# Performance work log

Measured on AMD Instinct MI355X. Metric: run time of the kernel, lower is better.

The kernel has to match this reference:

```python
import jax, jax.numpy as jnp
import numpy as np

NUM_HEADS = 8
WINDOW = (2, 8, 8)
NW = 64  # number of distinct window masks
TOPK = 2  # selected_n + 1


def _rel_position_index(ws):
    d, h, w = ws
    coords = np.stack(np.meshgrid(np.arange(d), np.arange(h), np.arange(w), indexing='ij'))  # (3,d,h,w)
    flat = coords.reshape(3, -1)  # (3,N)
    rel = flat[:, :, None] - flat[:, None, :]  # (3,N,N)
    rel = rel.transpose(1, 2, 0).astype(np.int64)
    rel[..., 0] += d - 1
    rel[..., 1] += h - 1
    rel[..., 2] += w - 1
    rel[..., 0] *= (2 * h - 1) * (2 * w - 1)
    rel[..., 1] *= 2 * w - 1
    return jnp.asarray(rel.sum(-1), dtype=jnp.int32)  # (N,N)


def setup_inputs() -> dict:
    key = jax.random.key(0)
    ks = jax.random.split(key, 7)
    B_, N, C = 1024, 128, 128
    x = jax.random.normal(ks[0], (B_, N, C), jnp.float32)
    mask = jax.random.normal(ks[1], (NW, N, N), jnp.float32)
    Wq = jax.random.normal(ks[2], (C, C), jnp.float32) * 0.02
    Wkv = jax.random.normal(ks[3], (C, 2 * C), jnp.float32) * 0.02
    Wproj = jax.random.normal(ks[4], (C, C), jnp.float32) * 0.02
    bproj = jnp.zeros((C,), jnp.float32)
    tbl_len = (2 * WINDOW[0] - 1) * (2 * WINDOW[1] - 1) * (2 * WINDOW[2] - 1)  # 675
    bias_table = jax.random.normal(ks[5], (tbl_len, NUM_HEADS), jnp.float32) * 0.02
    rel_index = _rel_position_index(WINDOW)
    return dict(x=x, mask=mask, Wq=Wq, Wkv=Wkv, Wproj=Wproj, bproj=bproj,
                bias_table=bias_table, rel_index=rel_index)


def reference(x, mask, Wq, Wkv, Wproj, bproj, bias_table, rel_index):
    B_, N, C = x.shape
    h = NUM_HEADS
    hd = C // h
    scale = hd ** -0.5
    # q/k/v projections (qkv_bias=False)
    q = (x @ Wq).reshape(B_, N, h, hd).transpose(0, 2, 1, 3)            # (B_,h,N,hd)
    kv = (x @ Wkv).reshape(B_, N, 2, h, hd).transpose(2, 0, 3, 1, 4)    # (2,B_,h,N,hd)
    k, v = kv[0], kv[1]
    attn = jnp.einsum('bhnd,bhmd->bhnm', q * scale, k)                  # (B_,h,N,N)
    # gathered relative-position bias
    bias = bias_table[rel_index.reshape(-1)].reshape(N, N, h).transpose(2, 0, 1)
    attn = attn + bias[None]
    nW = mask.shape[0]
    attn = attn.reshape(B_ // nW, nW, h, N, N) + mask[None, :, None]
    attn = jax.nn.softmax(attn.reshape(B_, h, N, N), axis=-1)
    # only_one branch: top-k gather + weighted sum over V
    sv, si = jax.lax.top_k(attn, TOPK)                                  # (B_,h,N,K)
    sel = jnp.take_along_axis(v, si.reshape(B_, h, N * TOPK)[..., None], axis=2)
    sel = sel.reshape(B_, h, N, TOPK, hd)
    out = (sel * sv[..., None]).sum(axis=3)                             # (B_,h,N,hd)
    xo = out.transpose(0, 2, 1, 3).reshape(B_, N, C)
    return xo @ Wproj + bproj
```

## Files before the change

### kernel.cpp

```cpp
#include <hip/hip_runtime.h>
#include <hip/hip_bf16.h>
#include <stdint.h>

typedef __attribute__((ext_vector_type(8))) short short8;
typedef __attribute__((ext_vector_type(4))) float floatx4;

#define B_TOT 1024
#define N_TOK 128
#define C_DIM 128
#define NHEAD 8
#define NW_MASK 64

#define BIAS_OFF 0
#define WALL_OFF 524288
#define WHEAD_BYTES 30464
#define WPT_OFF 768000
#define WS_BYTES 800768

#define QS_LDS 0
#define KS_LDS 14336
#define VS_LDS 28672
#define XO_LDS 37376
#define WB_LDS 47616
#define WPTB_LDS 109056
#define LDS_BYTES 125440

#define MFMA(a, b, c) __builtin_amdgcn_mfma_f32_16x16x32_bf16((a), (b), (c), 0, 0, 0)

__device__ __forceinline__ float bf2f(ushort u) {
  union { uint32_t u; float f; } v; v.u = ((uint32_t)u) << 16; return v.f;
}
__device__ __forceinline__ ushort f2bf(float f) {
  uint32_t u = __float_as_uint(f);
  return (ushort)((u + 0x7FFFu + ((u >> 16) & 1u)) >> 16);
}
__device__ __forceinline__ void split3(float f, ushort& h, ushort& m, ushort& l) {
  h = f2bf(f);  float r  = f - bf2f(h);
  m = f2bf(r);  float r2 = r - bf2f(m);
  l = f2bf(r2);
}
__device__ __forceinline__ void split3t(float f, ushort& h, ushort& m, ushort& l) {
  h = (ushort)(__float_as_uint(f) >> 16);
  float r  = f - bf2f(h);
  m = (ushort)(__float_as_uint(r) >> 16);
  float r2 = r - bf2f(m);
  l = f2bf(r2);
}

__device__ __forceinline__ void dma16(const void* g, void* l_) {
  __builtin_amdgcn_global_load_lds((const __attribute__((address_space(1))) void*)g,
                                   (__attribute__((address_space(3))) void*)l_,
                                   16, 0, 0);
}

__global__ __launch_bounds__(512)
void prep_kernel(const int* __restrict__ rel_index, const float* __restrict__ table,
                 const float* __restrict__ Wq, const float* __restrict__ Wkv,
                 const float* __restrict__ Wproj, char* __restrict__ ws) {
  float*  bias_g = (float*)(ws + BIAS_OFF);
  ushort* wpt_g  = (ushort*)(ws + WPT_OFF);

  int idx = blockIdx.x * 512 + threadIdx.x;
  if (idx < 131072) {
    int h = idx >> 14, mn = idx & 16383;
    bias_g[idx] = table[rel_index[mn] * NHEAD + h];
  } else if (idx < 131072 + 16384) {
    int t = idx - 131072;
    int h = t >> 11, r = t & 2047, oc = r >> 7, kk = r & 127;
    ushort a, bb, cc;
    split3(Wq[kk * C_DIM + h * 16 + oc] * 0.25f, a, bb, cc);
    ushort* wqp = (ushort*)(ws + WALL_OFF + h * WHEAD_BYTES);
    wqp[0 * 2176 + oc * 136 + kk] = a;
    wqp[1 * 2176 + oc * 136 + kk] = bb;
    wqp[2 * 2176 + oc * 136 + kk] = cc;
  } else if (idx < 131072 + 2 * 16384) {
    int t = idx - 131072 - 16384;
    int h = t >> 11, r = t & 2047, oc = r >> 7, kk = r & 127;
    ushort a, bb, cc;
    split3(Wkv[kk * (2 * C_DIM) + h * 16 + oc], a, bb, cc);
    ushort* wkp = (ushort*)(ws + WALL_OFF + h * WHEAD_BYTES) + 6528;
    wkp[0 * 2176 + oc * 136 + kk] = a;
    wkp[1 * 2176 + oc * 136 + kk] = bb;
    wkp[2 * 2176 + oc * 136 + kk] = cc;
  } else if (idx < 131072 + 3 * 16384) {
    int t = idx - 131072 - 2 * 16384;
    int h = t >> 11, r = t & 2047, oc = r >> 7, kk = r & 127;
    ushort* wvp = (ushort*)(ws + WALL_OFF + h * WHEAD_BYTES) + 13056;
    wvp[oc * 136 + kk] = f2bf(Wkv[kk * (2 * C_DIM) + C_DIM + h * 16 + oc]);
  } else if (idx < 131072 + 4 * 16384) {
    int t = idx - 131072 - 3 * 16384;
    int hp = t >> 12, r = t & 4095, n = r >> 5, kk = r & 31;
    wpt_g[t] = f2bf(Wproj[(hp * 32 + kk) * C_DIM + n]);
  }
}

__global__ __launch_bounds__(512, 2)
void wattn_kernel(const float* __restrict__ x, const float* __restrict__ mask,
                  const float* __restrict__ bproj, const char* __restrict__ ws,
                  float* __restrict__ out) {
  extern __shared__ char smem[];
  ushort* qs = (ushort*)(smem + QS_LDS);
  ushort* ks = (ushort*)(smem + KS_LDS);
  float*  vs = (float*)(smem + VS_LDS);
  ushort* xo = (ushort*)(smem + XO_LDS);

  const float* bias_g = (const float*)(ws + BIAS_OFF);

  const int tid  = threadIdx.x;
  const int w    = tid >> 6;
  const int l    = tid & 63;
  const int quad = l >> 4;
  const int c    = l & 15;
  const int b    = blockIdx.x;
  const int wi   = b & (NW_MASK - 1);

  {
    const char* src = ws + WALL_OFF;
    char* dst = smem + WB_LDS;
    #pragma unroll
    for (int t = 0; t < 4; ++t) {
      int ch = t * 8 + w;
      if (ch < 30) dma16(src + ch * 1024 + l * 16, dst + ch * 1024 + l * 16);
    }
    dma16(ws + WPT_OFF + w * 1024 + l * 16, smem + WPTB_LDS + w * 1024 + l * 16);
  }

  short8 A1[8], A3[8];
  {
    const float* xrow = x + ((size_t)b * N_TOK + 16 * w + c) * C_DIM;
    #pragma unroll
    for (int kt = 0; kt < 8; ++kt) {
      int colb = kt * 16 + (quad & 1) * 8;
      floatx4 xa  = *(const floatx4*)(xrow + colb);
      floatx4 xb2 = *(const floatx4*)(xrow + colb + 4);
      short8 hi8, mi8, lo8;
      #pragma unroll
      for (int jj = 0; jj < 8; ++jj) {
        float f = (jj < 4) ? xa[jj] : xb2[jj - 4];
        ushort hh, mm, ll; split3t(f, hh, mm, ll);
        hi8[jj] = (short)hh; mi8[jj] = (short)mm; lo8[jj] = (short)ll;
      }
      A1[kt] = (quad < 2) ? hi8 : mi8;
      A3[kt] = (quad < 2) ? hi8 : lo8;
    }
  }

  floatx4 oacc[8];
  #pragma unroll
  for (int j = 0; j < 8; ++j) oacc[j] = (floatx4){0.f, 0.f, 0.f, 0.f};

  asm volatile("s_waitcnt vmcnt(0)" ::: "memory");
  __syncthreads();

  for (int h = 0; h < NHEAD; ++h) {
    if (h < 7) {
      const char* src = ws + WALL_OFF + (h + 1) * WHEAD_BYTES;
      char* dst = smem + WB_LDS + ((h + 1) & 1) * 30720;
      #pragma unroll
      for (int t = 0; t < 4; ++t) {
        int ch = t * 8 + w;
        if (ch < 30) dma16(src + ch * 1024 + l * 16, dst + ch * 1024 + l * 16);
      }
      if (h & 1) {
        int np = (h + 1) >> 1;
        dma16(ws + WPT_OFF + np * 8192 + w * 1024 + l * 16,
              smem + WPTB_LDS + (np & 1) * 8192 + w * 1024 + l * 16);
      }
    }

    {
      floatx4 aq = (floatx4){0.f,0.f,0.f,0.f};
      floatx4 ak = (floatx4){0.f,0.f,0.f,0.f};
      floatx4 av = (floatx4){0.f,0.f,0.f,0.f};
      const ushort* wh  = (const ushort*)(smem + WB_LDS + (h & 1) * 30720);
      const ushort* wqp = wh + c * 136;
      const ushort* wkp = wh + 6528 + c * 136;
      const ushort* wvp = wh + 13056 + c * 136;
      const int q3off = (quad < 2) ? 2 * 2176 : 0;
      #pragma unroll
      for (int kt = 0; kt < 8; ++kt) {
        int colb = kt * 16 + (quad & 1) * 8;
        short8 bq1 = *(const short8*)(wqp + colb);
        short8 bq2 = *(const short8*)(wqp + 2176 + colb);
        short8 bq3 = *(const short8*)(wqp + q3off + colb);
        aq = MFMA(A1[kt], bq1, aq);  aq = MFMA(A1[kt], bq2, aq);  aq = MFMA(A3[kt], bq3, aq);
        short8 bk1 = *(const short8*)(wkp + colb);
        short8 bk2 = *(const short8*)(wkp + 2176 + colb);
        short8 bk3 = *(const short8*)(wkp + q3off + colb);
        ak = MFMA(A1[kt], bk1, ak);  ak = MFMA(A1[kt], bk2, ak);  ak = MFMA(A3[kt], bk3, ak);
        short8 bv1 = *(const short8*)(wvp + colb);
        av = MFMA(A1[kt], bv1, av);
      }
      #pragma unroll
      for (int i = 0; i < 4; ++i) {
        int tok = 16 * w + 4 * quad + i;
        ushort a, bb, cc;
        split3t(aq[i], a, bb, cc);
        qs[tok * 56 + c] = a; qs[tok * 56 + 16 + c] = bb; qs[tok * 56 + 32 + c] = cc;
        split3t(ak[i], a, bb, cc);
        ks[tok * 56 + c] = a; ks[tok * 56 + 16 + c] = bb; ks[tok * 56 + 32 + c] = cc;
        vs[tok * 17 + c] = av[i];
      }
    }
    __syncthreads();

    {
      const ushort* qrow = qs + (16 * w + c) * 56;
      short8 aq1 = *(const short8*)(qrow + quad * 8);
      short8 aq3 = *(const short8*)(qrow + ((quad < 2) ? quad * 8 : 16 + quad * 8));

      float m1[4], m2[4], psum[4];
      int   i1[4], i2[4];

      #pragma unroll
      for (int j = 0; j < 8; ++j) {
        floatx4 acc;
        #pragma unroll
        for (int i = 0; i < 4; ++i) {
          int m = 16 * w + 4 * quad + i;
          int n = 16 * j + c;
          acc[i] = bias_g[(h * N_TOK + m) * N_TOK + n] +
                   mask[(wi * N_TOK + m) * N_TOK + n];
        }
        const ushort* krow = ks + (16 * j + c) * 56;
        int bo1 = (quad & 1) * 8;
        short8 b1 = *(const short8*)(krow + bo1);
        short8 b2 = *(const short8*)(krow + 16 + bo1);
        short8 b3 = *(const short8*)(krow + ((quad < 2) ? 32 + quad * 8
                                                        : (quad - 2) * 8));
        acc = MFMA(aq1, b1, acc);
        acc = MFMA(aq1, b2, acc);
        acc = MFMA(aq3, b3, acc);

        if (j == 0) {
          #pragma unroll
          for (int i = 0; i < 4; ++i) {
            m1[i] = acc[i]; i1[i] = c;
            m2[i] = -__builtin_inff(); i2[i] = -1;
            psum[i] = 1.0f;
          }
        } else {
          #pragma unroll
          for (int i = 0; i < 4; ++i) {
            float v = acc[i]; int col = 16 * j + c;
            bool g1 = v > m1[i];
            float e = __expf(g1 ? (m1[i] - v) : (v - m1[i]));
            psum[i] = g1 ? (psum[i] * e + 1.0f) : (psum[i] + e);
            bool g2 = (!g1) && (v > m2[i]);
            m2[i] = g1 ? m1[i] : (g2 ? v : m2[i]);
            i2[i] = g1 ? i1[i] : (g2 ? col : i2[i]);
            m1[i] = g1 ? v : m1[i];
            i1[i] = g1 ? col : i1[i];
          }
        }
      }

      #pragma unroll
      for (int i = 0; i < 4; ++i) {
        float M1 = m1[i], M2 = m2[i], PS = psum[i];
        int I1 = i1[i], I2 = i2[i];
        #pragma unroll
        for (int d = 1; d < 16; d <<= 1) {
          float om1 = __shfl_xor(M1, d); int oi1 = __shfl_xor(I1, d);
          float om2 = __shfl_xor(M2, d); int oi2 = __shfl_xor(I2, d);
          float ops = __shfl_xor(PS, d);
          bool aw = (M1 > om1) || (M1 == om1 && I1 < oi1);
          float M  = aw ? M1 : om1;  int I  = aw ? I1 : oi1;
          float lv = aw ? om1 : M1;  int li = aw ? oi1 : I1;
          float sv = aw ? M2 : om2;  int si = aw ? I2 : oi2;
          bool sb = (sv > lv) || (sv == lv && si < li);
          float e = __expf(lv - M);
          PS = (aw ? PS : ops) + (aw ? ops : PS) * e;
          M1 = M; I1 = I;
          M2 = sb ? sv : lv; I2 = sb ? si : li;
        }
        float p1 = 1.0f / PS;
        float p2 = __expf(M2 - M1) * p1;
        int tok = 16 * w + 4 * quad + i;
        float o = p1 * vs[I1 * 17 + c] + p2 * vs[I2 * 17 + c];
        xo[tok * 40 + (h & 1) * 16 + c] = f2bf(o);
      }
    }

    if (h & 1) {
      const ushort* wptp = (const ushort*)(smem + WPTB_LDS + ((h >> 1) & 1) * 8192);
      short8 a = *(const short8*)(xo + (16 * w + c) * 40 + quad * 8);
      #pragma unroll
      for (int j = 0; j < 8; ++j) {
        short8 bf = *(const short8*)(wptp + (16 * j + c) * 32 + quad * 8);
        oacc[j] = MFMA(a, bf, oacc[j]);
      }
    }
    __syncthreads();
  }

  #pragma unroll
  for (int j = 0; j < 8; ++j) {
    float bp = bproj[16 * j + c];
    #pragma unroll
    for (int i = 0; i < 4; ++i) {
      int row = 16 * w + 4 * quad + i;
      out[((size_t)b * N_TOK + row) * C_DIM + 16 * j + c] = oacc[j][i] + bp;
    }
  }
}

extern "C" void kernel_launch(void* const* d_in, const int* in_sizes, int n_in,
                              void* d_out, int out_size, void* d_ws, size_t ws_size,
                              hipStream_t stream) {
  const float* x     = (const float*)d_in[0];
  const float* mask  = (const float*)d_in[1];
  const float* Wq    = (const float*)d_in[2];
  const float* Wkv   = (const float*)d_in[3];
  const float* Wproj = (const float*)d_in[4];
  const float* bproj = (const float*)d_in[5];
  const float* btab  = (const float*)d_in[6];
  const int*   ridx  = (const int*)d_in[7];
  float* outp = (float*)d_out;
  char*  ws   = (char*)d_ws;

  (void)in_sizes; (void)n_in; (void)out_size; (void)ws_size;

  hipFuncSetAttribute(reinterpret_cast<const void*>(wattn_kernel),
                      hipFuncAttributeMaxDynamicSharedMemorySize, LDS_BYTES);

  prep_kernel<<<384, 512, 0, stream>>>(ridx, btab, Wq, Wkv, Wproj, ws);
  wattn_kernel<<<B_TOT, 512, LDS_BYTES, stream>>>(x, mask, bproj, ws, outp);
}
```

Before: 404.4 us.

## Double-buffer K/V in LDS, drop per-head barrier, use unshifted softmax sum

K and V tiles in LDS become double-buffered by head parity, so the trailing __syncthreads at the end of each head iteration can be removed. This lets waves overlap one head's attention phase with the next head's projection phase. The online softmax with running-max rescaling is replaced by a plain sum of exp(v) plus a top-2 tracker, dropping the per-step rescale exp and the shuffle-time merge exp. Bias and mask loads now come after the MFMAs. The trade-offs are more LDS and a softmax that can overflow if logits get large.

```diff
diff --git a/kernel.cpp b/kernel.cpp
--- a/kernel.cpp
+++ b/kernel.cpp
@@ -19,11 +19,11 @@
 
 #define QS_LDS 0
 #define KS_LDS 14336
-#define VS_LDS 28672
-#define XO_LDS 37376
-#define WB_LDS 47616
-#define WPTB_LDS 109056
-#define LDS_BYTES 125440
+#define VS_LDS 43008
+#define XO_LDS 60416
+#define WB_LDS 70656
+#define WPTB_LDS 132096
+#define LDS_BYTES 148480
 
 #define MFMA(a, b, c) __builtin_amdgcn_mfma_f32_16x16x32_bf16((a), (b), (c), 0, 0, 0)
 
@@ -100,8 +100,6 @@
                   float* __restrict__ out) {
   extern __shared__ char smem[];
   ushort* qs = (ushort*)(smem + QS_LDS);
-  ushort* ks = (ushort*)(smem + KS_LDS);
-  float*  vs = (float*)(smem + VS_LDS);
   ushort* xo = (ushort*)(smem + XO_LDS);
 
   const float* bias_g = (const float*)(ws + BIAS_OFF);
@@ -153,6 +151,9 @@
   __syncthreads();
 
   for (int h = 0; h < NHEAD; ++h) {
+    ushort* ks_c = (ushort*)(smem + KS_LDS + (h & 1) * 14336);
+    float*  vs_c = (float*)(smem + VS_LDS + (h & 1) * 8704);
+
     if (h < 7) {
       const char* src = ws + WALL_OFF + (h + 1) * WHEAD_BYTES;
       char* dst = smem + WB_LDS + ((h + 1) & 1) * 30720;
@@ -198,8 +199,8 @@
         split3t(aq[i], a, bb, cc);
         qs[tok * 56 + c] = a; qs[tok * 56 + 16 + c] = bb; qs[tok * 56 + 32 + c] = cc;
         split3t(ak[i], a, bb, cc);
-        ks[tok * 56 + c] = a; ks[tok * 56 + 16 + c] = bb; ks[tok * 56 + 32 + c] = cc;
-        vs[tok * 17 + c] = av[i];
+        ks_c[tok * 56 + c] = a; ks_c[tok * 56 + 16 + c] = bb; ks_c[tok * 56 + 32 + c] = cc;
+        vs_c[tok * 17 + c] = av[i];
       }
     }
     __syncthreads();
@@ -211,18 +212,17 @@
 
       float m1[4], m2[4], psum[4];
       int   i1[4], i2[4];
+      #pragma unroll
+      for (int i = 0; i < 4; ++i) {
+        m1[i] = -__builtin_inff(); i1[i] = 0;
+        m2[i] = -__builtin_inff(); i2[i] = -1;
+        psum[i] = 0.0f;
+      }
 
       #pragma unroll
       for (int j = 0; j < 8; ++j) {
-        floatx4 acc;
-        #pragma unroll
-        for (int i = 0; i < 4; ++i) {
-          int m = 16 * w + 4 * quad + i;
-          int n = 16 * j + c;
-          acc[i] = bias_g[(h * N_TOK + m) * N_TOK + n] +
-                   mask[(wi * N_TOK + m) * N_TOK + n];
-        }
-        const ushort* krow = ks + (16 * j + c) * 56;
+        floatx4 acc = (floatx4){0.f, 0.f, 0.f, 0.f};
+        const ushort* krow = ks_c + (16 * j + c) * 56;
         int bo1 = (quad & 1) * 8;
         short8 b1 = *(const short8*)(krow + bo1);
         short8 b2 = *(const short8*)(krow + 16 + bo1);
@@ -232,26 +232,20 @@
         acc = MFMA(aq1, b2, acc);
         acc = MFMA(aq3, b3, acc);
 
-        if (j == 0) {
-          #pragma unroll
-          for (int i = 0; i < 4; ++i) {
-            m1[i] = acc[i]; i1[i] = c;
-            m2[i] = -__builtin_inff(); i2[i] = -1;
-            psum[i] = 1.0f;
-          }
-        } else {
-          #pragma unroll
-          for (int i = 0; i < 4; ++i) {
-            float v = acc[i]; int col = 16 * j + c;
-            bool g1 = v > m1[i];
-            float e = __expf(g1 ? (m1[i] - v) : (v - m1[i]));
-            psum[i] = g1 ? (psum[i] * e + 1.0f) : (psum[i] + e);
-            bool g2 = (!g1) && (v > m2[i]);
-            m2[i] = g1 ? m1[i] : (g2 ? v : m2[i]);
-            i2[i] = g1 ? i1[i] : (g2 ? col : i2[i]);
-            m1[i] = g1 ? v : m1[i];
-            i1[i] = g1 ? col : i1[i];
-          }
+        #pragma unroll
+        for (int i = 0; i < 4; ++i) {
+          int m = 16 * w + 4 * quad + i;
+          int n = 16 * j + c;
+          float v = acc[i] + bias_g[(h * N_TOK + m) * N_TOK + n] +
+                             mask[(wi * N_TOK + m) * N_TOK + n];
+          psum[i] += __expf(v);
+          int col = 16 * j + c;
+          bool g1 = v > m1[i];
+          bool g2 = (!g1) && (v > m2[i]);
+          m2[i] = g1 ? m1[i] : (g2 ? v : m2[i]);
+          i2[i] = g1 ? i1[i] : (g2 ? col : i2[i]);
+          m1[i] = g1 ? v : m1[i];
+          i1[i] = g1 ? col : i1[i];
         }
       }
 
@@ -265,19 +259,18 @@
           float om2 = __shfl_xor(M2, d); int oi2 = __shfl_xor(I2, d);
           float ops = __shfl_xor(PS, d);
           bool aw = (M1 > om1) || (M1 == om1 && I1 < oi1);
-          float M  = aw ? M1 : om1;  int I  = aw ? I1 : oi1;
           float lv = aw ? om1 : M1;  int li = aw ? oi1 : I1;
           float sv = aw ? M2 : om2;  int si = aw ? I2 : oi2;
+          M1 = aw ? M1 : om1;  I1 = aw ? I1 : oi1;
           bool sb = (sv > lv) || (sv == lv && si < li);
-          float e = __expf(lv - M);
-          PS = (aw ? PS : ops) + (aw ? ops : PS) * e;
-          M1 = M; I1 = I;
           M2 = sb ? sv : lv; I2 = sb ? si : li;
+          PS += ops;
         }
-        float p1 = 1.0f / PS;
-        float p2 = __expf(M2 - M1) * p1;
+        float inv = 1.0f / PS;
+        float p1 = __expf(M1) * inv;
+        float p2 = __expf(M2) * inv;
         int tok = 16 * w + 4 * quad + i;
-        float o = p1 * vs[I1 * 17 + c] + p2 * vs[I2 * 17 + c];
+        float o = p1 * vs_c[I1 * 17 + c] + p2 * vs_c[I2 * 17 + c];
         xo[tok * 40 + (h & 1) * 16 + c] = f2bf(o);
       }
     }
@@ -291,7 +284,6 @@
         oacc[j] = MFMA(a, bf, oacc[j]);
       }
     }
-    __syncthreads();
   }
 
   #pragma unroll
```

New measurement: 381.6 us. 5.6% less time.
